# Performance work log

Hardware: AMD Instinct MI355X
Metric: run time of the kernel (lower is better)

## Reference

```python
import jax, jax.numpy as jnp
import numpy as np

B, G, NPA, NT, L = 8192, 689, 16, 131, 6
S = G + NPA * NT  # 2785 = 689 genes + 16 nodes per each of 131 assemblies


def setup_inputs() -> dict:
    key = jax.random.key(0)
    ks = jax.random.split(key, 8)
    x = jax.random.normal(ks[0], (B, G), dtype=jnp.float32)
    # depth-0 mask: place the 689 gene inputs into the first 689 slots of the layer
    lm0 = jnp.zeros((G, S), jnp.float32).at[jnp.arange(G), jnp.arange(G)].set(1.0)
    # per-depth sparse binary connectivity masks (ontology DAG edges at each depth)
    lm = (jax.random.uniform(ks[1], (L, S, S)) < 0.02).astype(jnp.float32)
    # diagonal pass-through masks for edges skipping this depth (stored as diagonals)
    flm_diag = (jax.random.uniform(ks[2], (L, S)) < 0.3).astype(jnp.float32)
    # final assembly selector: the nodes_per_assembly slots of the root assembly
    fasm = jnp.zeros((S,), jnp.float32).at[G:G + NPA].set(1.0)
    W0 = jax.random.normal(ks[3], (G, S), dtype=jnp.float32) * 0.05
    b0 = jnp.zeros((S,), jnp.float32)
    W = jax.random.normal(ks[4], (L, S, S), dtype=jnp.float32) * 0.05
    b = jnp.zeros((L, S), jnp.float32)
    gamma = jnp.ones((L + 1, S), jnp.float32)
    beta = jnp.zeros((L + 1, S), jnp.float32)
    w_out = jax.random.normal(ks[5], (S,), dtype=jnp.float32) * 0.05
    b_out = jnp.zeros((), jnp.float32)
    return {"x": x, "lm0": lm0, "lm": lm, "flm_diag": flm_diag, "fasm": fasm,
            "W0": W0, "b0": b0, "W": W, "b": b, "gamma": gamma, "beta": beta,
            "w_out": w_out, "b_out": b_out}


def _bn(h, g, bt, eps=1e-5):
    # training-mode BatchNorm1d over the batch axis
    m = h.mean(axis=0)
    v = h.var(axis=0)
    return (h - m) * jax.lax.rsqrt(v + eps) * g + bt


def reference(x, lm0, lm, flm_diag, fasm, W0, b0, W, b, gamma, beta, w_out, b_out):
    # depth 0: masked linear placing genes into layer slots, BN before activation
    h = jnp.tanh(_bn(x @ (W0 * lm0) + b0, gamma[0], beta[0]))  # [B, S]
    def step(h, layer):
        Wl, bl, lml, dl, gl, btl = layer
        # masked linear + BN + activation, plus diagonal pass-through skip
        hn = jnp.tanh(_bn(h @ (Wl * lml) + bl, gl, btl)) + h * dl
        return hn, None
    h, _ = jax.lax.scan(step, h, (W, b, lm, flm_diag, gamma[1:], beta[1:]))
    # output_method='final': linear head on final-assembly nodes only
    return (h * fasm) @ w_out + b_out  # [B]
```

## Files before the change

### kernel.cpp

```cpp
#include <hip/hip_runtime.h>
#include <hip/hip_fp16.h>
#include <stdint.h>

typedef uint32_t u32;
typedef uint64_t u64;
typedef unsigned int v4u __attribute__((ext_vector_type(4)));
typedef float v4f __attribute__((ext_vector_type(4)));

constexpr int CB   = 8192;
constexpr int CG   = 689;
constexpr int CL   = 6;
constexpr int CS   = 2785;
constexpr int CSP  = 2816;
constexpr int CRS  = 8256;
constexpr int KCAP = 112;

union V16 { v4u u; __half2 h2[4]; };
union F4  { v4f v; float f[4]; u32 u[4]; };

__global__ __launch_bounds__(256) void build_main(const float* __restrict__ lm,
                                                  const float* __restrict__ W,
                                                  u64* __restrict__ ent,
                                                  int* __restrict__ cnt)
{
    const int total = CL * CS * CS;
    int base = (blockIdx.x * 256 + threadIdx.x) * 16;
#pragma unroll
    for (int c = 0; c < 4; c++) {
        int i4 = base + c * 4;
        if (i4 >= total) return;
        F4 m4;
        bool full = (i4 + 4 <= total);
        if (full) {
            m4.v = __builtin_nontemporal_load(reinterpret_cast<const v4f*>(lm + i4));
        } else {
            for (int q = 0; q < 4; q++) m4.f[q] = (i4 + q < total) ? lm[i4 + q] : 0.f;
        }
        if ((m4.u[0] | m4.u[1] | m4.u[2] | m4.u[3]) == 0u) continue;
        F4 w4;
        if (full) {
            w4.v = *reinterpret_cast<const v4f*>(W + i4);
        } else {
            for (int q = 0; q < 4; q++) w4.f[q] = (i4 + q < total) ? W[i4 + q] : 0.f;
        }
#pragma unroll
        for (int q = 0; q < 4; q++) {
            if (m4.f[q] != 0.0f) {
                int i = i4 + q;
                int s = i % CS;
                int r = i / CS;
                int l = r / CS;
                int j = r % CS;
                int col = l * CSP + s;
                int pos = atomicAdd(&cnt[col], 1);
                if (pos < KCAP) {
                    u32 off = (u32)j * (u32)(CRS * 2);
                    ent[(size_t)col * KCAP + pos] = ((u64)off << 32) | (u64)__float_as_uint(w4.f[q]);
                }
            }
        }
    }
}

__global__ __launch_bounds__(256) void build0(const float* __restrict__ lm0,
                                              const float* __restrict__ W0,
                                              u64* __restrict__ ent,
                                              int* __restrict__ cnt)
{
    const int total = CG * CS;
    int i4 = (blockIdx.x * 256 + threadIdx.x) * 4;
    if (i4 >= total) return;
    float mm[4], ww[4];
    if (i4 + 4 <= total) {
        float4 m4 = *reinterpret_cast<const float4*>(lm0 + i4);
        float4 w4 = *reinterpret_cast<const float4*>(W0 + i4);
        mm[0]=m4.x; mm[1]=m4.y; mm[2]=m4.z; mm[3]=m4.w;
        ww[0]=w4.x; ww[1]=w4.y; ww[2]=w4.z; ww[3]=w4.w;
    } else {
        for (int q = 0; q < 4; q++) {
            mm[q] = (i4 + q < total) ? lm0[i4 + q] : 0.f;
            ww[q] = (i4 + q < total) ? W0[i4 + q]  : 0.f;
        }
    }
#pragma unroll
    for (int q = 0; q < 4; q++) {
        if (mm[q] != 0.0f) {
            int i = i4 + q;
            int s = i % CS;
            int j = i / CS;
            int pos = atomicAdd(&cnt[s], 1);
            if (pos < KCAP) {
                u32 off = (u32)j * (u32)(CRS * 2);
                ent[(size_t)s * KCAP + pos] = ((u64)off << 32) | (u64)__float_as_uint(ww[q]);
            }
        }
    }
}

__global__ __launch_bounds__(256) void transpose_x(const float* __restrict__ x,
                                                   __half* __restrict__ xT)
{
    __shared__ float tile[32][33];
    int gx = blockIdx.x * 32;
    int gy = blockIdx.y * 32;
    int tx = threadIdx.x, ty = threadIdx.y;
#pragma unroll
    for (int i = 0; i < 32; i += 8) {
        int g = gx + tx;
        int b = gy + ty + i;
        tile[ty + i][tx] = (g < CG) ? x[(size_t)b * CG + g] : 0.f;
    }
    __syncthreads();
#pragma unroll
    for (int i = 0; i < 32; i += 8) {
        int g = gx + ty + i;
        int b = gy + tx;
        if (g < CG) xT[(size_t)g * CRS + b] = __float2half(tile[tx][ty + i]);
    }
}

__global__ __launch_bounds__(64) void gather_k(const __half* __restrict__ src,
                                               __half* __restrict__ dst,
                                               const u64* __restrict__ ent,
                                               const int* __restrict__ cnt,
                                               const float* __restrict__ bias,
                                               float* __restrict__ sumv,
                                               float* __restrict__ sumq,
                                               int boff0)
{
    int s    = blockIdx.y;
    int lane = threadIdx.x;
    int boff = boff0 + blockIdx.x * 512 + lane * 8;

    int n = cnt[s]; if (n > KCAP) n = KCAP;
    int ng = (n + 7) >> 3;
    const u64* e = ent + (size_t)s * KCAP;
    const char* sb = (const char*)src + (size_t)boff * 2;

    float bv = bias[s];
    float acc[8];
#pragma unroll
    for (int j = 0; j < 8; j++) acc[j] = bv;

    for (int g = 0; g < ng; g++) {
        u64 ev[8];
#pragma unroll
        for (int q = 0; q < 8; q++) ev[q] = e[g * 8 + q];
        V16 rv[8];
#pragma unroll
        for (int q = 0; q < 8; q++)
            rv[q].u = *reinterpret_cast<const v4u*>(sb + (u32)(ev[q] >> 32));
#pragma unroll
        for (int q = 0; q < 8; q++) {
            float w = __uint_as_float((u32)(ev[q] & 0xffffffffu));
#pragma unroll
            for (int j = 0; j < 4; j++) {
                float2 f = __half22float2(rv[q].h2[j]);
                acc[2*j]   = fmaf(w, f.x, acc[2*j]);
                acc[2*j+1] = fmaf(w, f.y, acc[2*j+1]);
            }
        }
    }

    V16 o;
#pragma unroll
    for (int j = 0; j < 4; j++) o.h2[j] = __floats2half2_rn(acc[2*j], acc[2*j+1]);
    __builtin_nontemporal_store(o.u, reinterpret_cast<v4u*>(dst + (size_t)s * CRS + boff));

    float ls = 0.f, lq = 0.f;
#pragma unroll
    for (int j = 0; j < 8; j++) { ls += acc[j]; lq += acc[j] * acc[j]; }
#pragma unroll
    for (int off = 32; off > 0; off >>= 1) {
        ls += __shfl_xor(ls, off);
        lq += __shfl_xor(lq, off);
    }
    if (lane == 0) { atomicAdd(&sumv[s], ls); atomicAdd(&sumq[s], lq); }
}

__global__ __launch_bounds__(64) void bn_act(__half* __restrict__ h,
                                             const __half* __restrict__ prev,
                                             const float* __restrict__ sumv,
                                             const float* __restrict__ sumq,
                                             const float* __restrict__ gamma,
                                             const float* __restrict__ beta,
                                             const float* __restrict__ dlv)
{
    int s = blockIdx.y;
    int boff = blockIdx.x * 512 + threadIdx.x * 8;
    float mean = sumv[s] * (1.0f / CB);
    float var  = sumq[s] * (1.0f / CB) - mean * mean;
    float rstd = rsqrtf(var + 1e-5f);
    float scale = gamma[s] * rstd;
    float shift = beta[s] - mean * scale;
    size_t base = (size_t)s * CRS + boff;
    V16 v; v.u = *reinterpret_cast<const v4u*>(h + base);
    V16 pv;
    float d = 0.f;
    if (prev) { d = dlv[s]; pv.u = *reinterpret_cast<const v4u*>(prev + base); }
    V16 o;
#pragma unroll
    for (int j = 0; j < 4; j++) {
        float2 f = __half22float2(v.h2[j]);
        float t0 = tanhf(fmaf(f.x, scale, shift));
        float t1 = tanhf(fmaf(f.y, scale, shift));
        if (prev) {
            float2 p = __half22float2(pv.h2[j]);
            t0 = fmaf(d, p.x, t0);
            t1 = fmaf(d, p.y, t1);
        }
        o.h2[j] = __floats2half2_rn(t0, t1);
    }
    *reinterpret_cast<v4u*>(h + base) = o.u;
}

__global__ __launch_bounds__(256) void head_prep(const float* __restrict__ fasm,
                                                 const float* __restrict__ wout,
                                                 int* __restrict__ hcnt,
                                                 int* __restrict__ hs,
                                                 float* __restrict__ hc)
{
    int s = blockIdx.x * 256 + threadIdx.x;
    if (s >= CS) return;
    float c = fasm[s] * wout[s];
    if (c != 0.f) {
        int p = atomicAdd(hcnt, 1);
        if (p < 64) { hs[p] = s; hc[p] = c; }
    }
}

__global__ __launch_bounds__(256) void head_k(const __half* __restrict__ h,
                                              const int* __restrict__ hcnt,
                                              const int* __restrict__ hs,
                                              const float* __restrict__ hc,
                                              const float* __restrict__ bout,
                                              float* __restrict__ out)
{
    int b = blockIdx.x * 256 + threadIdx.x;
    int n = *hcnt; if (n > 64) n = 64;
    float acc = bout[0];
    for (int k = 0; k < n; k++) {
        int s = hs[k];
        float c = hc[k];
        acc = fmaf(c, __half2float(h[(size_t)s * CRS + b]), acc);
    }
    out[b] = acc;
}

extern "C" void kernel_launch(void* const* d_in, const int* in_sizes, int n_in,
                              void* d_out, int out_size, void* d_ws, size_t ws_size,
                              hipStream_t stream)
{
    const float* x    = (const float*)d_in[0];
    const float* lm0  = (const float*)d_in[1];
    const float* lm   = (const float*)d_in[2];
    const float* flm  = (const float*)d_in[3];
    const float* fasm = (const float*)d_in[4];
    const float* W0   = (const float*)d_in[5];
    const float* b0   = (const float*)d_in[6];
    const float* W    = (const float*)d_in[7];
    const float* bb   = (const float*)d_in[8];
    const float* gam  = (const float*)d_in[9];
    const float* bet  = (const float*)d_in[10];
    const float* wout = (const float*)d_in[11];
    const float* bout = (const float*)d_in[12];
    float* out = (float*)d_out;

    char* ws = (char*)d_ws;
    int*    cnt  = (int*)ws;
    float*  sumv = (float*)(ws + 78848);
    float*  sumq = (float*)(ws + 157696);
    int*    hcnt = (int*)(ws + 236544);
    int*    hs   = (int*)(ws + 236560);
    float*  hc   = (float*)(ws + 236816);
    u64*    ent  = (u64*)(ws + 237184);
    __half* hA   = (__half*)(ws + 17899136);
    __half* hB   = (__half*)(ws + 63885056);
    __half* xT   = hB;

    (void)hipMemsetAsync(ws, 0, 17899136, stream);

    { int total = CL * CS * CS; build_main<<<dim3((total + 4095) / 4096), 256, 0, stream>>>(lm, W, ent + (size_t)CSP * KCAP, cnt + CSP); }
    { int total = CG * CS;      build0   <<<dim3((total + 1023) / 1024), 256, 0, stream>>>(lm0, W0, ent, cnt); }
    transpose_x<<<dim3(22, 256), dim3(32, 8), 0, stream>>>(x, xT);
    head_prep<<<dim3(11), 256, 0, stream>>>(fasm, wout, hcnt, hs, hc);

    const __half* cur = xT;
    __half* bufs[2] = {hA, hB};
    int which = 0;
    for (int t = 0; t < 7; t++) {
        __half* dst = bufs[which];
        const float* bias = (t == 0) ? b0 : bb + (size_t)(t - 1) * CS;
        for (int half = 0; half < 2; half++) {
            gather_k<<<dim3(8, CS), 64, 0, stream>>>(cur, dst,
                ent + (size_t)t * CSP * KCAP, cnt + t * CSP, bias,
                sumv + t * CSP, sumq + t * CSP, half * 4096);
        }
        bn_act<<<dim3(16, CS), 64, 0, stream>>>(dst, (t == 0) ? nullptr : cur,
            sumv + t * CSP, sumq + t * CSP, gam + (size_t)t * CS, bet + (size_t)t * CS,
            (t == 0) ? nullptr : flm + (size_t)(t - 1) * CS);
        cur = dst;
        which ^= 1;
    }
    head_k<<<dim3(32), 256, 0, stream>>>(cur, hcnt, hs, hc, bout, out);
}
```

Baseline: 1.400 ms.

## Compute last layer only for head-selected nodes and restructure sparse-build kernels

The final depth now gathers only the nodes that feed the output head (selected via the head_prep list), and the last BN plus tanh plus skip are fused into the head kernel. This avoids computing and storing all 2785 columns at the last layer. The build kernels are reorganised to one block per mask row, and weights are stored as fp16 in the entry table. The two half-batch gather launches are merged into a single launch using grid z. Storing weights as fp16 loses weight precision, and the 16-block launch assumes at most 16 head nodes.

```diff
diff --git a/kernel.cpp b/kernel.cpp
--- a/kernel.cpp
+++ b/kernel.cpp
@@ -6,6 +6,7 @@
 typedef uint64_t u64;
 typedef unsigned int v4u __attribute__((ext_vector_type(4)));
 typedef float v4f __attribute__((ext_vector_type(4)));
+typedef _Float16 v2h __attribute__((ext_vector_type(2)));
 
 constexpr int CB   = 8192;
 constexpr int CG   = 689;
@@ -15,47 +16,48 @@
 constexpr int CRS  = 8256;
 constexpr int KCAP = 112;
 
-union V16 { v4u u; __half2 h2[4]; };
+union V16 { v4u u; v2h h2[4]; };
 union F4  { v4f v; float f[4]; u32 u[4]; };
+union HW  { u32 u; v2h h; };
 
 __global__ __launch_bounds__(256) void build_main(const float* __restrict__ lm,
                                                   const float* __restrict__ W,
                                                   u64* __restrict__ ent,
                                                   int* __restrict__ cnt)
 {
-    const int total = CL * CS * CS;
-    int base = (blockIdx.x * 256 + threadIdx.x) * 16;
-#pragma unroll
-    for (int c = 0; c < 4; c++) {
-        int i4 = base + c * 4;
-        if (i4 >= total) return;
-        F4 m4;
-        bool full = (i4 + 4 <= total);
-        if (full) {
-            m4.v = __builtin_nontemporal_load(reinterpret_cast<const v4f*>(lm + i4));
+    int rb = blockIdx.x;
+    int l  = rb / CS;
+    int j  = rb - l * CS;
+    const float* lrow = lm + (size_t)rb * CS;
+    const float* wrow = W  + (size_t)rb * CS;
+    u64 hi = ((u64)((u32)j * (u32)(CRS * 2))) << 32;
+    int colbase = l * CSP;
+
+    for (int s4 = threadIdx.x * 4; s4 < CS; s4 += 1024) {
+        if (s4 + 4 <= CS) {
+            F4 m4; m4.v = *reinterpret_cast<const v4f*>(lrow + s4);
+            if ((m4.u[0] | m4.u[1] | m4.u[2] | m4.u[3]) == 0u) continue;
+            F4 w4; w4.v = *reinterpret_cast<const v4f*>(wrow + s4);
+#pragma unroll
+            for (int q = 0; q < 4; q++) {
+                if (m4.f[q] != 0.0f) {
+                    int s = s4 + q;
+                    int pos = atomicAdd(&cnt[colbase + s], 1);
+                    if (pos < KCAP) {
+                        u32 hw = (u32)__half_as_ushort(__float2half(w4.f[q]));
+                        ent[(size_t)(colbase + s) * KCAP + pos] = hi | (u64)(hw | (hw << 16));
+                    }
+                }
+            }
         } else {
-            for (int q = 0; q < 4; q++) m4.f[q] = (i4 + q < total) ? lm[i4 + q] : 0.f;
-        }
-        if ((m4.u[0] | m4.u[1] | m4.u[2] | m4.u[3]) == 0u) continue;
-        F4 w4;
-        if (full) {
-            w4.v = *reinterpret_cast<const v4f*>(W + i4);
-        } else {
-            for (int q = 0; q < 4; q++) w4.f[q] = (i4 + q < total) ? W[i4 + q] : 0.f;
-        }
-#pragma unroll
-        for (int q = 0; q < 4; q++) {
-            if (m4.f[q] != 0.0f) {
-                int i = i4 + q;
-                int s = i % CS;
-                int r = i / CS;
-                int l = r / CS;
-                int j = r % CS;
-                int col = l * CSP + s;
-                int pos = atomicAdd(&cnt[col], 1);
-                if (pos < KCAP) {
-                    u32 off = (u32)j * (u32)(CRS * 2);
-                    ent[(size_t)col * KCAP + pos] = ((u64)off << 32) | (u64)__float_as_uint(w4.f[q]);
+            for (int s = s4; s < CS; s++) {
+                float m = lrow[s];
+                if (m != 0.0f) {
+                    int pos = atomicAdd(&cnt[colbase + s], 1);
+                    if (pos < KCAP) {
+                        u32 hw = (u32)__half_as_ushort(__float2half(wrow[s]));
+                        ent[(size_t)(colbase + s) * KCAP + pos] = hi | (u64)(hw | (hw << 16));
+                    }
                 }
             }
         }
@@ -67,31 +69,36 @@
                                               u64* __restrict__ ent,
                                               int* __restrict__ cnt)
 {
-    const int total = CG * CS;
-    int i4 = (blockIdx.x * 256 + threadIdx.x) * 4;
-    if (i4 >= total) return;
-    float mm[4], ww[4];
-    if (i4 + 4 <= total) {
-        float4 m4 = *reinterpret_cast<const float4*>(lm0 + i4);
-        float4 w4 = *reinterpret_cast<const float4*>(W0 + i4);
-        mm[0]=m4.x; mm[1]=m4.y; mm[2]=m4.z; mm[3]=m4.w;
-        ww[0]=w4.x; ww[1]=w4.y; ww[2]=w4.z; ww[3]=w4.w;
-    } else {
-        for (int q = 0; q < 4; q++) {
-            mm[q] = (i4 + q < total) ? lm0[i4 + q] : 0.f;
-            ww[q] = (i4 + q < total) ? W0[i4 + q]  : 0.f;
-        }
-    }
-#pragma unroll
-    for (int q = 0; q < 4; q++) {
-        if (mm[q] != 0.0f) {
-            int i = i4 + q;
-            int s = i % CS;
-            int j = i / CS;
-            int pos = atomicAdd(&cnt[s], 1);
-            if (pos < KCAP) {
-                u32 off = (u32)j * (u32)(CRS * 2);
-                ent[(size_t)s * KCAP + pos] = ((u64)off << 32) | (u64)__float_as_uint(ww[q]);
+    int j = blockIdx.x;
+    const float* lrow = lm0 + (size_t)j * CS;
+    const float* wrow = W0  + (size_t)j * CS;
+    u64 hi = ((u64)((u32)j * (u32)(CRS * 2))) << 32;
+    for (int s4 = threadIdx.x * 4; s4 < CS; s4 += 1024) {
+        if (s4 + 4 <= CS) {
+            F4 m4; m4.v = *reinterpret_cast<const v4f*>(lrow + s4);
+            if ((m4.u[0] | m4.u[1] | m4.u[2] | m4.u[3]) == 0u) continue;
+            F4 w4; w4.v = *reinterpret_cast<const v4f*>(wrow + s4);
+#pragma unroll
+            for (int q = 0; q < 4; q++) {
+                if (m4.f[q] != 0.0f) {
+                    int s = s4 + q;
+                    int pos = atomicAdd(&cnt[s], 1);
+                    if (pos < KCAP) {
+                        u32 hw = (u32)__half_as_ushort(__float2half(w4.f[q]));
+                        ent[(size_t)s * KCAP + pos] = hi | (u64)(hw | (hw << 16));
+                    }
+                }
+            }
+        } else {
+            for (int s = s4; s < CS; s++) {
+                float m = lrow[s];
+                if (m != 0.0f) {
+                    int pos = atomicAdd(&cnt[s], 1);
+                    if (pos < KCAP) {
+                        u32 hw = (u32)__half_as_ushort(__float2half(wrow[s]));
+                        ent[(size_t)s * KCAP + pos] = hi | (u64)(hw | (hw << 16));
+                    }
+                }
             }
         }
     }
@@ -126,11 +133,18 @@
                                                const float* __restrict__ bias,
                                                float* __restrict__ sumv,
                                                float* __restrict__ sumq,
-                                               int boff0)
-{
-    int s    = blockIdx.y;
+                                               const int* __restrict__ sel,
+                                               const int* __restrict__ selcnt)
+{
+    int s;
+    if (sel) {
+        if ((int)blockIdx.y >= *selcnt) return;
+        s = sel[blockIdx.y];
+    } else {
+        s = blockIdx.y;
+    }
     int lane = threadIdx.x;
-    int boff = boff0 + blockIdx.x * 512 + lane * 8;
+    int boff = blockIdx.z * 4096 + blockIdx.x * 512 + lane * 8;
 
     int n = cnt[s]; if (n > KCAP) n = KCAP;
     int ng = (n + 7) >> 3;
@@ -152,10 +166,16 @@
             rv[q].u = *reinterpret_cast<const v4u*>(sb + (u32)(ev[q] >> 32));
 #pragma unroll
         for (int q = 0; q < 8; q++) {
-            float w = __uint_as_float((u32)(ev[q] & 0xffffffffu));
+            HW w2; w2.u = (u32)ev[q];
 #pragma unroll
             for (int j = 0; j < 4; j++) {
-                float2 f = __half22float2(rv[q].h2[j]);
+                float2 a2;
+                a2.x = acc[2*j]; a2.y = acc[2*j+1];
+#if __has_builtin(__builtin_amdgcn_fdot2)
+#endif
+                (void)a2;
+                float2 f = __half22float2(*(const __half2*)&rv[q].h2[j]);
+                float w = __half2float(*(const __half*)&w2.h);
                 acc[2*j]   = fmaf(w, f.x, acc[2*j]);
                 acc[2*j+1] = fmaf(w, f.y, acc[2*j+1]);
             }
@@ -164,7 +184,10 @@
 
     V16 o;
 #pragma unroll
-    for (int j = 0; j < 4; j++) o.h2[j] = __floats2half2_rn(acc[2*j], acc[2*j+1]);
+    for (int j = 0; j < 4; j++) {
+        v2h p; p.x = (_Float16)acc[2*j]; p.y = (_Float16)acc[2*j+1];
+        o.h2[j] = p;
+    }
     __builtin_nontemporal_store(o.u, reinterpret_cast<v4u*>(dst + (size_t)s * CRS + boff));
 
     float ls = 0.f, lq = 0.f;
@@ -201,15 +224,16 @@
     V16 o;
 #pragma unroll
     for (int j = 0; j < 4; j++) {
-        float2 f = __half22float2(v.h2[j]);
+        float2 f = __half22float2(*(const __half2*)&v.h2[j]);
         float t0 = tanhf(fmaf(f.x, scale, shift));
         float t1 = tanhf(fmaf(f.y, scale, shift));
         if (prev) {
-            float2 p = __half22float2(pv.h2[j]);
+            float2 p = __half22float2(*(const __half2*)&pv.h2[j]);
             t0 = fmaf(d, p.x, t0);
             t1 = fmaf(d, p.y, t1);
         }
-        o.h2[j] = __floats2half2_rn(t0, t1);
+        v2h pk; pk.x = (_Float16)t0; pk.y = (_Float16)t1;
+        o.h2[j] = pk;
     }
     *reinterpret_cast<v4u*>(h + base) = o.u;
 }
@@ -229,10 +253,16 @@
     }
 }
 
-__global__ __launch_bounds__(256) void head_k(const __half* __restrict__ h,
+__global__ __launch_bounds__(256) void head_k(const __half* __restrict__ h6pre,
+                                              const __half* __restrict__ h5,
                                               const int* __restrict__ hcnt,
                                               const int* __restrict__ hs,
                                               const float* __restrict__ hc,
+                                              const float* __restrict__ sumv,
+                                              const float* __restrict__ sumq,
+                                              const float* __restrict__ gamma,
+                                              const float* __restrict__ beta,
+                                              const float* __restrict__ dlv,
                                               const float* __restrict__ bout,
                                               float* __restrict__ out)
 {
@@ -241,8 +271,15 @@
     float acc = bout[0];
     for (int k = 0; k < n; k++) {
         int s = hs[k];
-        float c = hc[k];
-        acc = fmaf(c, __half2float(h[(size_t)s * CRS + b]), acc);
+        float mean = sumv[s] * (1.0f / CB);
+        float var  = sumq[s] * (1.0f / CB) - mean * mean;
+        float rstd = rsqrtf(var + 1e-5f);
+        float scale = gamma[s] * rstd;
+        float shift = beta[s] - mean * scale;
+        float pre  = __half2float(h6pre[(size_t)s * CRS + b]);
+        float prev = __half2float(h5[(size_t)s * CRS + b]);
+        float hn = tanhf(fmaf(pre, scale, shift)) + dlv[s] * prev;
+        acc = fmaf(hc[k], hn, acc);
     }
     out[b] = acc;
 }
@@ -280,27 +317,31 @@
 
     (void)hipMemsetAsync(ws, 0, 17899136, stream);
 
-    { int total = CL * CS * CS; build_main<<<dim3((total + 4095) / 4096), 256, 0, stream>>>(lm, W, ent + (size_t)CSP * KCAP, cnt + CSP); }
-    { int total = CG * CS;      build0   <<<dim3((total + 1023) / 1024), 256, 0, stream>>>(lm0, W0, ent, cnt); }
+    build_main<<<dim3(CL * CS), 256, 0, stream>>>(lm, W, ent + (size_t)CSP * KCAP, cnt + CSP);
+    build0    <<<dim3(CG),      256, 0, stream>>>(lm0, W0, ent, cnt);
     transpose_x<<<dim3(22, 256), dim3(32, 8), 0, stream>>>(x, xT);
     head_prep<<<dim3(11), 256, 0, stream>>>(fasm, wout, hcnt, hs, hc);
 
     const __half* cur = xT;
     __half* bufs[2] = {hA, hB};
     int which = 0;
-    for (int t = 0; t < 7; t++) {
+    for (int t = 0; t < 6; t++) {
         __half* dst = bufs[which];
         const float* bias = (t == 0) ? b0 : bb + (size_t)(t - 1) * CS;
-        for (int half = 0; half < 2; half++) {
-            gather_k<<<dim3(8, CS), 64, 0, stream>>>(cur, dst,
-                ent + (size_t)t * CSP * KCAP, cnt + t * CSP, bias,
-                sumv + t * CSP, sumq + t * CSP, half * 4096);
-        }
+        gather_k<<<dim3(8, CS, 2), 64, 0, stream>>>(cur, dst,
+            ent + (size_t)t * CSP * KCAP, cnt + t * CSP, bias,
+            sumv + t * CSP, sumq + t * CSP, nullptr, nullptr);
         bn_act<<<dim3(16, CS), 64, 0, stream>>>(dst, (t == 0) ? nullptr : cur,
             sumv + t * CSP, sumq + t * CSP, gam + (size_t)t * CS, bet + (size_t)t * CS,
             (t == 0) ? nullptr : flm + (size_t)(t - 1) * CS);
         cur = dst;
         which ^= 1;
     }
-    head_k<<<dim3(32), 256, 0, stream>>>(cur, hcnt, hs, hc, bout, out);
-}
+    __half* h6 = bufs[which];
+    gather_k<<<dim3(8, 16, 2), 64, 0, stream>>>(cur, h6,
+        ent + (size_t)6 * CSP * KCAP, cnt + 6 * CSP, bb + (size_t)5 * CS,
+        sumv + 6 * CSP, sumq + 6 * CSP, hs, hcnt);
+    head_k<<<dim3(32), 256, 0, stream>>>(h6, cur, hcnt, hs, hc,
+        sumv + 6 * CSP, sumq + 6 * CSP, gam + (size_t)6 * CS, bet + (size_t)6 * CS,
+        flm + (size_t)5 * CS, bout, out);
+}
```

Result: faster. 1.197 ms (-14.5%).
